# Kernel tuning notes

Measured on AMD Instinct MI355X. Metric: run time of the kernel, lower is better.

## Reference

```python
import jax, jax.numpy as jnp
import numpy as np

# hyperparameters (match init_kwargs)
LS = 0.2; GAMMA = 2.0; THING_W = 2.0; L_DB = 0.1; SIGMA = 0.05; TEMP = 0.1
L_DISTILL = 1.0; L_BPL = 0.5; L_ALIGN = 5.0; L_PROTO = 0.5; L_ENT = 0.3
L_IU = 0.5; L_IB = 0.5
MIN_PIX = 25; NUM_IDS = 24  # instance ids in [0, NUM_IDS)


def setup_inputs() -> dict:
    key = jax.random.key(0)
    k0, k1, k2, k3, k4 = jax.random.split(key, 5)
    B, C, H, W, D = 4, 27, 160, 160, 768
    return {
        "logits": jax.random.normal(k0, (B, C, H, W), jnp.float32),
        "cause_logits": jax.random.normal(k1, (B, C, H, W), jnp.float32),
        "dinov2_features": jax.random.normal(k2, (B, D, H, W), jnp.float32),
        "depth": jax.random.uniform(k3, (B, 1, H, W), jnp.float32),
        "instance_map": jax.random.randint(k4, (B, 1, H, W), 0, NUM_IDS),
    }


def _bce(x, y):
    x = jnp.clip(x, 1e-6, 1.0 - 1e-6)
    return -(y * jnp.log(x) + (1.0 - y) * jnp.log1p(-x)).mean()


def _forward(logits, cause_logits, dinov2_features, depth, instance_map):
    B, C, H, W = logits.shape
    logp = jax.nn.log_softmax(logits, axis=1)
    probs = jnp.exp(logp)

    # ---- distill: label-smoothed CE vs CAUSE hard labels, focal + thing + depth-boundary weights
    cause_labels = jnp.argmax(cause_logits, axis=1)  # (B,H,W)
    nll = -jnp.take_along_axis(logp, cause_labels[:, None], axis=1)[:, 0]  # (B,H,W)
    ce = (1.0 - LS) * nll + LS * (-logp.mean(axis=1))
    pt = jnp.exp(-jax.lax.stop_gradient(ce))
    w = (1.0 - pt) ** GAMMA
    thing = (cause_labels >= 11) & (cause_labels <= 18)
    w = jnp.where(thing, w * THING_W, w)
    gh = jnp.pad(jnp.abs(depth[:, :, 1:, :] - depth[:, :, :-1, :]), ((0, 0), (0, 0), (0, 1), (0, 0)))
    gw = jnp.pad(jnp.abs(depth[:, :, :, 1:] - depth[:, :, :, :-1]), ((0, 0), (0, 0), (0, 0), (0, 1)))
    gmag = (gh + gw)[:, 0]  # (B,H,W)
    gnorm = gmag / (gmag.mean() + 1e-6)
    w = w * (1.0 + L_DB * jnp.minimum(gnorm, 3.0))
    l_distill = (ce * w).mean()

    # ---- boundary preservation loss (CE re-weighted at pseudo-label boundaries)
    pl = jnp.pad(cause_labels, ((0, 0), (1, 1), (1, 1)), mode="edge")
    boundary = ((cause_labels != pl[:, 1:-1, 2:]) | (cause_labels != pl[:, 1:-1, :-2]) |
                (cause_labels != pl[:, 2:, 1:-1]) | (cause_labels != pl[:, :-2, 1:-1])).astype(jnp.float32)
    bsum = boundary.sum()
    l_bpl = jnp.where(bsum > 0, (ce * boundary).sum() / jnp.maximum(bsum, 1.0), 0.0)

    # ---- depth-boundary alignment
    two_s2 = 2.0 * SIGMA ** 2
    ddh = jnp.abs(depth[:, :, :, 1:] - depth[:, :, :, :-1])
    wh = jnp.exp(-(ddh ** 2) / two_s2)
    pdh = ((probs[:, :, :, 1:] - probs[:, :, :, :-1]) ** 2).sum(axis=1, keepdims=True)
    ddv = jnp.abs(depth[:, :, 1:, :] - depth[:, :, :-1, :])
    wv = jnp.exp(-(ddv ** 2) / two_s2)
    pdv = ((probs[:, :, 1:, :] - probs[:, :, :-1, :]) ** 2).sum(axis=1, keepdims=True)
    l_align = (wh * pdh).mean() + (wv * pdv).mean()

    # ---- feature prototype loss
    N = H * W
    probs_t = jax.nn.softmax(logits / TEMP, axis=1).reshape(B, C, N)   # (B,C,N)
    feats = dinov2_features.reshape(B, -1, N)                          # (B,D,N)
    protos = jnp.einsum("bdn,bcn->bdc", feats, probs_t)               # (B,D,C)
    wsum = probs_t.sum(axis=2)[:, None, :]                             # (B,1,C)
    protos = protos / (wsum + 1e-6)
    protos_n = protos / jnp.maximum(jnp.linalg.norm(protos, axis=1, keepdims=True), 1e-12)
    feats_n = feats / jnp.maximum(jnp.linalg.norm(feats, axis=1, keepdims=True), 1e-12)
    sim = jnp.einsum("bdc,bdn->bcn", protos_n, feats_n)               # (B,C,N)
    l_proto = -(probs_t * sim).sum() / (B * N)

    # ---- entropy loss
    l_ent = -(probs * logp).sum(axis=1).mean()

    # ---- instance boundary loss
    dh = jnp.abs(probs[:, :, 1:, :] - probs[:, :, :-1, :]).max(axis=1)
    dw = jnp.abs(probs[:, :, :, 1:] - probs[:, :, :, :-1]).max(axis=1)
    inst = instance_map[:, 0].astype(jnp.float32)
    th = (inst[:, 1:, :] != inst[:, :-1, :]).astype(jnp.float32)
    tw = (inst[:, :, 1:] != inst[:, :, :-1]).astype(jnp.float32)
    l_ib = (_bce(dh, th) + _bce(dw, tw)) / 2.0

    # ---- instance uniformity loss (vectorized segment reduce over instance ids)
    ids = instance_map[:, 0].reshape(B, N)                             # (B,N) int
    onehot = (ids[:, :, None] == jnp.arange(NUM_IDS)[None, None, :]).astype(jnp.float32)  # (B,N,K)
    counts = onehot.sum(axis=1)                                        # (B,K)
    pf = probs.reshape(B, C, N)
    s1 = jnp.einsum("bcn,bnk->bkc", pf, onehot)                       # per-id sum of probs
    s2 = jnp.einsum("bcn,bnk->bkc", pf * pf, onehot)                  # per-id sum of probs^2
    nc = jnp.maximum(counts, 1.0)[:, :, None]
    var = (s2 / nc - (s1 / nc) ** 2).mean(axis=2)                     # (B,K): mean over C of within-id variance
    valid = ((jnp.arange(NUM_IDS)[None, :] > 0) & (counts >= MIN_PIX)).astype(jnp.float32)
    l_iu = (var * valid).sum() / jnp.maximum(valid.sum(), 1.0)

    total = (L_DISTILL * l_distill + L_BPL * l_bpl + L_ALIGN * l_align +
             L_PROTO * l_proto + L_ENT * l_ent + L_IU * l_iu + L_IB * l_ib)
    return total


def reference(logits, cause_logits, dinov2_features, depth, instance_map):
    return _forward(logits, cause_logits, dinov2_features, depth, instance_map)
```

## Files before the change

### kernel.cpp

```cpp
#include <hip/hip_runtime.h>
#include <cstdint>
#include <cstddef>

#define BN 4
#define CC 27
#define HH 160
#define WW 160
#define HWp (HH*WW)
#define NPIX (BN*HWp)
#define DD 768
#define KK 24
#define NT 400
#define NTS 20
#define NSP 20
#define NPH (NTS/2)
#define GEMMB (BN*6*NSP)
#define TAILB (NPIX/256)

#define OFF_ACC 0
#define OFF_S1 32
#define OFF_S2 (OFF_S1+2592)
#define OFF_CNT (OFF_S2+2592)
#define ZERO_N (OFF_CNT+96)
#define OFF_NSQ8 ZERO_N
#define OFF_LAB (OFF_NSQ8 + 8*NPIX)
#define OFF_PROBS (OFF_LAB + NPIX/4)
#define OFF_PP (OFF_PROBS + BN*CC*HWp/2)
#define OFF_QP (OFF_PP + NSP*BN*CC*DD)
#define OFF_FBF (OFF_QP + NSP*BN*CC*DD)
#define OFF_WBF (OFF_FBF + (size_t)BN*6*NT*8192/4)

typedef __attribute__((ext_vector_type(4))) float f32x4;

__device__ __forceinline__ float wave_sum(float v) {
#pragma unroll
  for (int o = 32; o > 0; o >>= 1) v += __shfl_down(v, o, 64);
  return v;
}

__device__ __forceinline__ unsigned char f2fp8(float x) {
  return (unsigned char)(__builtin_amdgcn_cvt_pk_fp8_f32(x, x, 0, false) & 0xff);
}
__device__ __forceinline__ unsigned short f2bf(float x) {
  unsigned u = __builtin_bit_cast(unsigned, x);
  unsigned r = u + 0x7FFFu + ((u >> 16) & 1u);
  return (unsigned short)(r >> 16);
}
__device__ __forceinline__ float bf2f(unsigned short u) {
  unsigned v = ((unsigned)u) << 16;
  return __builtin_bit_cast(float, v);
}

__global__ void k_zero(float* __restrict__ w, int n) {
  int i = blockIdx.x * 256 + threadIdx.x;
  if (i < n) w[i] = 0.f;
}

__global__ void __launch_bounds__(256) k_prefconv(const float* __restrict__ feats,
        const float* __restrict__ depth, const float* __restrict__ cl,
        unsigned char* __restrict__ fbf, float* __restrict__ nsq8,
        unsigned char* __restrict__ lab, float* __restrict__ acc) {
  int t = threadIdx.x;
  if (blockIdx.x < 800) {
    int fcid = blockIdx.x;
    int slab = fcid % 100;
    int y = fcid / 100;
    int b = slab / (HWp / 1024);
    int px0 = (slab % (HWp / 1024)) * 1024;
    int d0 = y * (DD / 8);
    int p = px0 + 4 * t;
    int T = p >> 6, j = p & 63;
    const float* src = feats + ((size_t)b * DD + d0) * HWp + p;
    float n0 = 0.f, n1 = 0.f, n2 = 0.f, n3 = 0.f;
#pragma unroll 4
    for (int d = 0; d < DD / 8; ++d) {
      int dgl = d0 + d;
      float4 v = *(const float4*)(src + (size_t)d * HWp);
      n0 += v.x * v.x; n1 += v.y * v.y; n2 += v.z * v.z; n3 += v.w * v.w;
      int pk = __builtin_amdgcn_cvt_pk_fp8_f32(v.x, v.y, 0, false);
      pk = __builtin_amdgcn_cvt_pk_fp8_f32(v.z, v.w, pk, true);
      int dt = dgl >> 7, rin = dgl & 127;
      size_t addr = ((size_t)(b * 6 + dt) * NT + T) * 8192 + rin * 64
                  + (((j >> 3) ^ (rin & 7)) * 8) + (j & 7);
      *(int*)&fbf[addr] = pk;
    }
    float* nq = nsq8 + (size_t)y * NPIX + b * HWp + p;
    nq[0] = n0; nq[1] = n1; nq[2] = n2; nq[3] = n3;
  } else {
    int i = (blockIdx.x - 800) * 256 + t;
    float g = 0.f;
    {
      int b = i / HWp, r = i % HWp, h = r / WW, w = r % WW;
      const float* dp = depth + b * HWp;
      float d0 = dp[r];
      float gh = (h < HH-1) ? fabsf(dp[r+WW] - d0) : 0.f;
      float gw = (w < WW-1) ? fabsf(dp[r+1] - d0) : 0.f;
      g = gh + gw;
      const float* p = cl + (size_t)b * CC * HWp + r;
      float best = p[0]; int bi = 0;
#pragma unroll
      for (int c = 1; c < CC; ++c) {
        float v = p[(size_t)c * HWp];
        if (v > best) { best = v; bi = c; }
      }
      lab[i] = (unsigned char)bi;
    }
    __shared__ float red;
    if (t == 0) red = 0.f;
    __syncthreads();
    float s = wave_sum(g);
    if ((t & 63) == 0) atomicAdd(&red, s);
    __syncthreads();
    if (t == 0) atomicAdd(&acc[0], red);
  }
}

__global__ void k_main(const float* __restrict__ logits, const float* __restrict__ depth,
                       const unsigned char* __restrict__ lab, const float* __restrict__ nsq8,
                       unsigned short* __restrict__ probs, unsigned char* __restrict__ wbf,
                       float* __restrict__ acc) {
  int i = blockIdx.x * 256 + threadIdx.x;
  float c_dist = 0.f, c_bnum = 0.f, c_bcnt = 0.f, c_ent = 0.f;
  {
    int b = i / HWp, r = i % HWp, h = r / WW, w = r % WW;
    const float* lg = logits + (size_t)b * CC * HWp + r;
    float x[CC];
    float m = -1e30f;
#pragma unroll
    for (int c = 0; c < CC; ++c) { x[c] = lg[(size_t)c * HWp]; m = fmaxf(m, x[c]); }
    float se = 0.f, sx = 0.f, set = 0.f;
#pragma unroll
    for (int c = 0; c < CC; ++c) {
      se += expf(x[c] - m);
      set += expf(10.f * (x[c] - m));
      sx += x[c];
    }
    float lse = logf(se);
    float inv_set = 1.f / set;
    float ns = 0.f;
#pragma unroll
    for (int y = 0; y < 8; ++y) ns += nsq8[(size_t)y * NPIX + i];
    float invn = 1.f / fmaxf(sqrtf(ns), 1e-12f);
    int l = lab[i];
    float xl = x[0];
    float ent = 0.f;
    unsigned short* pb = probs + (size_t)b * CC * HWp + r;
    int T = r >> 6, j = r & 63;
    unsigned char* wb = wbf + ((size_t)b * NT + T) * 4096;
#pragma unroll
    for (int c = 0; c < CC; ++c) {
      float lp = x[c] - m - lse;
      float p = expf(lp);
      pb[(size_t)c * HWp] = f2bf(p);
      float ptc = expf(10.f * (x[c] - m)) * inv_set;
      wb[c * 64 + (((j >> 3) ^ (c & 7)) * 8) + (j & 7)] = f2fp8(ptc);
      int c2 = 32 + c;
      wb[c2 * 64 + (((j >> 3) ^ (c2 & 7)) * 8) + (j & 7)] = f2fp8(ptc * invn);
      ent -= p * lp;
      if (c == l) xl = x[c];
    }
    float nll = m + lse - xl;
    float ce = 0.8f * nll + 0.2f * (m + lse - sx * (1.f / CC));
    float ptf = expf(-ce);
    float wgt = (1.f - ptf) * (1.f - ptf);
    if (l >= 11 && l <= 18) wgt *= 2.f;
    const float* dp = depth + b * HWp;
    float d0 = dp[r];
    float gh = (h < HH-1) ? fabsf(dp[r+WW] - d0) : 0.f;
    float gw = (w < WW-1) ? fabsf(dp[r+1] - d0) : 0.f;
    float gmean = acc[0] * (1.f / NPIX);
    float gnorm = (gh + gw) / (gmean + 1e-6f);
    wgt *= 1.f + 0.1f * fminf(gnorm, 3.f);
    const unsigned char* lb = lab + b * HWp;
    int lL = lb[h*WW + (w>0 ? w-1 : w)];
    int lR = lb[h*WW + (w<WW-1 ? w+1 : w)];
    int lU = lb[(h>0 ? h-1 : h)*WW + w];
    int lD = lb[(h<HH-1 ? h+1 : h)*WW + w];
    float bnd = ((l != lL) | (l != lR) | (l != lU) | (l != lD)) ? 1.f : 0.f;
    c_dist = ce * wgt;
    c_bnum = ce * bnd;
    c_bcnt = bnd;
    c_ent = ent;
  }
  __shared__ float red[4];
  if (threadIdx.x < 4) red[threadIdx.x] = 0.f;
  __syncthreads();
  c_dist = wave_sum(c_dist); c_bnum = wave_sum(c_bnum);
  c_bcnt = wave_sum(c_bcnt); c_ent = wave_sum(c_ent);
  if ((threadIdx.x & 63) == 0) {
    atomicAdd(&red[0], c_dist); atomicAdd(&red[1], c_bnum);
    atomicAdd(&red[2], c_bcnt); atomicAdd(&red[3], c_ent);
  }
  __syncthreads();
  if (threadIdx.x == 0) {
    atomicAdd(&acc[1], red[0]); atomicAdd(&acc[2], red[1]);
    atomicAdd(&acc[3], red[2]); atomicAdd(&acc[4], red[3]);
  }
}

__global__ void __launch_bounds__(256) k_gemmtail(const unsigned char* __restrict__ fbf,
        const unsigned char* __restrict__ wbf,
        float* __restrict__ Pp, float* __restrict__ Qp,
        const unsigned short* __restrict__ probs, const float* __restrict__ depth,
        const int* __restrict__ inst, float* __restrict__ acc,
        float* __restrict__ s1g, float* __restrict__ s2g, float* __restrict__ cntg) {
  __shared__ __align__(16) unsigned char smem[73728];
  int t = threadIdx.x;
  if (blockIdx.x < GEMMB) {
    unsigned char (*As)[2][8192] = (unsigned char (*)[2][8192])smem;
    unsigned char (*Ws)[2][4096] = (unsigned char (*)[2][4096])(smem + 49152);
    int orig = blockIdx.x;
    int bx = (orig & 7) * 60 + (orig >> 3);
    int s  = bx % NSP;
    int dt = (bx / NSP) % 6;
    int b  = bx / (NSP * 6);
    int wave = t >> 6, lane = t & 63;
    int g = lane >> 4, rr = lane & 15;
    f32x4 acc4[2][4] = {};
    const unsigned char* Abase = fbf + ((size_t)(b*6+dt)*NT + s*NTS) * 8192;
    const unsigned char* Wbase = wbf + ((size_t)b*NT + s*NTS) * 4096;

#define STAGE2(ph, bufi) do { \
    _Pragma("unroll") \
    for (int c2_ = 0; c2_ < 2; ++c2_) { \
      const unsigned char* as_ = Abase + (size_t)((ph)*2 + c2_) * 8192; \
      const unsigned char* ws_ = Wbase + (size_t)((ph)*2 + c2_) * 4096; \
      _Pragma("unroll") \
      for (int i_ = 0; i_ < 2; ++i_) { \
        int off_ = wave*2048 + i_*1024; \
        __builtin_amdgcn_global_load_lds( \
          (const __attribute__((address_space(1))) void*)(as_ + off_ + lane*16), \
          (__attribute__((address_space(3))) void*)&As[bufi][c2_][off_], 16, 0, 0); \
      } \
      { \
        int off_ = wave*1024; \
        __builtin_amdgcn_global_load_lds( \
          (const __attribute__((address_space(1))) void*)(ws_ + off_ + lane*16), \
          (__attribute__((address_space(3))) void*)&Ws[bufi][c2_][off_], 16, 0, 0); \
      } \
    } \
  } while (0)

    STAGE2(0, 0);
    STAGE2(1, 1);
    int cur = 0;
    for (int ph = 0; ph < NPH; ++ph) {
      if (ph + 2 < NPH) {
        STAGE2(ph + 2, (cur + 2) % 3);
        asm volatile("s_waitcnt vmcnt(12)" ::: "memory");
      } else if (ph + 1 < NPH) {
        asm volatile("s_waitcnt vmcnt(6)" ::: "memory");
      } else {
        asm volatile("s_waitcnt vmcnt(0)" ::: "memory");
      }
      __builtin_amdgcn_s_barrier();
      __builtin_amdgcn_sched_barrier(0);
#pragma unroll
      for (int c2 = 0; c2 < 2; ++c2) {
#pragma unroll
        for (int ks = 0; ks < 2; ++ks) {
          long a[2]; long wf[4];
#pragma unroll
          for (int dd = 0; dd < 2; ++dd) {
            int row = (wave*2 + dd)*16 + rr;
            int ck = (ks*4 + g) ^ (row & 7);
            a[dd] = *(const long*)&As[cur][c2][row*64 + ck*8];
          }
#pragma unroll
          for (int ct = 0; ct < 4; ++ct) {
            int row = ct*16 + rr;
            int ck = (ks*4 + g) ^ (row & 7);
            wf[ct] = *(const long*)&Ws[cur][c2][row*64 + ck*8];
          }
#pragma unroll
          for (int dd = 0; dd < 2; ++dd)
#pragma unroll
            for (int ct = 0; ct < 4; ++ct)
              acc4[dd][ct] = __builtin_amdgcn_mfma_f32_16x16x32_fp8_fp8(a[dd], wf[ct], acc4[dd][ct], 0, 0, 0);
        }
      }
      __builtin_amdgcn_sched_barrier(0);
      __builtin_amdgcn_s_barrier();
      cur = (cur + 1) % 3;
    }
#undef STAGE2
#pragma unroll
    for (int dd = 0; dd < 2; ++dd) {
#pragma unroll
      for (int ct = 0; ct < 4; ++ct) {
        int cp = ct * 16 + rr;
        int d = dt * 128 + (wave * 2 + dd) * 16 + g * 4;
        f32x4 v = acc4[dd][ct];
        if (cp < CC)
          *(f32x4*)&Pp[(((size_t)s * BN + b) * CC + cp) * DD + d] = v;
        else if (cp >= 32 && cp < 32 + CC)
          *(f32x4*)&Qp[(((size_t)s * BN + b) * CC + (cp - 32)) * DD + d] = v;
      }
    }
  } else {
    float* ls1 = (float*)smem;
    float* ls2 = ls1 + 4*KK*CC;
    float* lc  = ls2 + 4*KK*CC;
    float* red = lc + 4*KK;
    int wv = t >> 6;
    for (int idx = t; idx < 4*KK*CC; idx += 256) { ls1[idx] = 0.f; ls2[idx] = 0.f; }
    if (t < 4*KK) lc[t] = 0.f;
    if (t < 4) red[t] = 0.f;
    __syncthreads();
    int i = (blockIdx.x - GEMMB) * 256 + t;
    int b = i / HWp, r = i % HWp, h = r / WW, w = r % WW;
    const unsigned short* P = probs + (size_t)b * CC * HWp + r;
    const int* ip = inst + b * HWp;
    int id = ip[r];
    atomicAdd(&lc[wv*KK + id], 1.f);
    bool hasR = (w < WW-1), hasD = (h < HH-1);
    float sh = 0.f, sv = 0.f, mh = 0.f, mw = 0.f;
#pragma unroll
    for (int c = 0; c < CC; ++c) {
      float p  = bf2f(P[(size_t)c * HWp]);
      atomicAdd(&ls1[(wv*KK + id)*CC + c], p);
      atomicAdd(&ls2[(wv*KK + id)*CC + c], p * p);
      float pr = hasR ? bf2f(P[(size_t)c * HWp + 1])  : p;
      float pd = hasD ? bf2f(P[(size_t)c * HWp + WW]) : p;
      float dr = pr - p, dd = pd - p;
      sh += dr * dr; sv += dd * dd;
      mw = fmaxf(mw, fabsf(dr)); mh = fmaxf(mh, fabsf(dd));
    }
    float aH = 0.f, aV = 0.f, bh = 0.f, bw = 0.f;
    const float* dp = depth + b * HWp;
    float d0 = dp[r];
    if (hasR) {
      float ddh = dp[r+1] - d0;
      aH = expf(-(ddh*ddh) * 200.f) * sh;
      float y = (ip[r+1] != ip[r]) ? 1.f : 0.f;
      float xx = fminf(fmaxf(mw, 1e-6f), 1.f - 1e-6f);
      bw = -(y * logf(xx) + (1.f - y) * log1pf(-xx));
    }
    if (hasD) {
      float ddv = dp[r+WW] - d0;
      aV = expf(-(ddv*ddv) * 200.f) * sv;
      float y = (ip[r+WW] != ip[r]) ? 1.f : 0.f;
      float xx = fminf(fmaxf(mh, 1e-6f), 1.f - 1e-6f);
      bh = -(y * logf(xx) + (1.f - y) * log1pf(-xx));
    }
    __syncthreads();
    aH = wave_sum(aH); aV = wave_sum(aV); bh = wave_sum(bh); bw = wave_sum(bw);
    if ((t & 63) == 0) {
      atomicAdd(&red[0], aH); atomicAdd(&red[1], aV);
      atomicAdd(&red[2], bh); atomicAdd(&red[3], bw);
    }
    __syncthreads();
    if (t == 0) {
      atomicAdd(&acc[5], red[0]); atomicAdd(&acc[6], red[1]);
      atomicAdd(&acc[7], red[2]); atomicAdd(&acc[8], red[3]);
    }
    for (int idx = t; idx < KK*CC; idx += 256) {
      atomicAdd(&s1g[b*KK*CC + idx], ls1[idx]+ls1[KK*CC+idx]+ls1[2*KK*CC+idx]+ls1[3*KK*CC+idx]);
      atomicAdd(&s2g[b*KK*CC + idx], ls2[idx]+ls2[KK*CC+idx]+ls2[2*KK*CC+idx]+ls2[3*KK*CC+idx]);
    }
    if (t < KK) atomicAdd(&cntg[b*KK + t], lc[t]+lc[KK+t]+lc[2*KK+t]+lc[3*KK+t]);
  }
}

__global__ void k_pfinal(const float* __restrict__ Pp, const float* __restrict__ Qp,
                         float* __restrict__ acc) {
  int bc = blockIdx.x;
  int b = bc / CC, c = bc % CC;
  float dot = 0.f, nsq = 0.f;
  for (int d = threadIdx.x; d < DD; d += 256) {
    float p = 0.f, q = 0.f;
#pragma unroll
    for (int s = 0; s < NSP; ++s) {
      size_t off = (((size_t)s * BN + b) * CC + c) * DD + d;
      p += Pp[off]; q += Qp[off];
    }
    dot += p * q; nsq += p * p;
  }
  __shared__ float red[2];
  if (threadIdx.x < 2) red[threadIdx.x] = 0.f;
  __syncthreads();
  dot = wave_sum(dot); nsq = wave_sum(nsq);
  if ((threadIdx.x & 63) == 0) { atomicAdd(&red[0], dot); atomicAdd(&red[1], nsq); }
  __syncthreads();
  if (threadIdx.x == 0) atomicAdd(&acc[9], red[0] / fmaxf(sqrtf(red[1]), 1e-12f));
}

__global__ void k_final(const float* __restrict__ s1g, const float* __restrict__ s2g,
                        const float* __restrict__ cntg, const float* __restrict__ acc,
                        float* __restrict__ out) {
  int t = threadIdx.x;
  float vsum = 0.f, vcnt = 0.f;
  if (t < BN*KK) {
    int k = t % KK;
    float count = cntg[t];
    float nc = fmaxf(count, 1.f);
    float var = 0.f;
#pragma unroll
    for (int c = 0; c < CC; ++c) {
      float m1 = s1g[t*CC + c] / nc;
      var += s2g[t*CC + c] / nc - m1 * m1;
    }
    var *= (1.f / CC);
    if (k > 0 && count >= 25.f) { vsum = var; vcnt = 1.f; }
  }
  __shared__ float red[2];
  if (t < 2) red[t] = 0.f;
  __syncthreads();
  vsum = wave_sum(vsum); vcnt = wave_sum(vcnt);
  if ((t & 63) == 0) { atomicAdd(&red[0], vsum); atomicAdd(&red[1], vcnt); }
  __syncthreads();
  if (t == 0) {
    float l_distill = acc[1] * (1.f / NPIX);
    float bcnt = acc[3];
    float l_bpl = (bcnt > 0.f) ? acc[2] / fmaxf(bcnt, 1.f) : 0.f;
    float l_align = acc[5] * (1.f / (BN*HH*(WW-1))) + acc[6] * (1.f / (BN*(HH-1)*WW));
    float l_ent = acc[4] * (1.f / NPIX);
    float l_ib = 0.5f * (acc[7] * (1.f / (BN*(HH-1)*WW)) + acc[8] * (1.f / (BN*HH*(WW-1))));
    float l_proto = -acc[9] * (1.f / NPIX);
    float l_iu = red[0] / fmaxf(red[1], 1.f);
    out[0] = 1.0f*l_distill + 0.5f*l_bpl + 5.0f*l_align + 0.5f*l_proto +
             0.3f*l_ent + 0.5f*l_iu + 0.5f*l_ib;
  }
}

extern "C" void kernel_launch(void* const* d_in, const int* in_sizes, int n_in,
                              void* d_out, int out_size, void* d_ws, size_t ws_size,
                              hipStream_t stream) {
  (void)in_sizes; (void)n_in; (void)out_size; (void)ws_size;
  const float* logits = (const float*)d_in[0];
  const float* cause  = (const float*)d_in[1];
  const float* feats  = (const float*)d_in[2];
  const float* depth  = (const float*)d_in[3];
  const int*   inst   = (const int*)d_in[4];
  float* ws = (float*)d_ws;
  float* acc = ws + OFF_ACC;
  float* s1  = ws + OFF_S1;
  float* s2  = ws + OFF_S2;
  float* cnt = ws + OFF_CNT;
  float* nsq8 = ws + OFF_NSQ8;
  float* Pp  = ws + OFF_PP;
  float* Qp  = ws + OFF_QP;
  unsigned char* lab = (unsigned char*)(ws + OFF_LAB);
  unsigned short* probs = (unsigned short*)(ws + OFF_PROBS);
  unsigned char* fbf = (unsigned char*)(ws + OFF_FBF);
  unsigned char* wbf = (unsigned char*)(ws + OFF_WBF);
  float* out = (float*)d_out;

  k_zero<<<(ZERO_N + 255) / 256, 256, 0, stream>>>(ws, ZERO_N);
  k_prefconv<<<1200, 256, 0, stream>>>(feats, depth, cause, fbf, nsq8, lab, acc);
  k_main<<<NPIX / 256, 256, 0, stream>>>(logits, depth, lab, nsq8, probs, wbf, acc);
  k_gemmtail<<<GEMMB + TAILB, 256, 0, stream>>>(fbf, wbf, Pp, Qp, probs, depth, inst,
                                                acc, s1, s2, cnt);
  k_pfinal<<<BN * CC, 256, 0, stream>>>(Pp, Qp, acc);
  k_final<<<1, 256, 0, stream>>>(s1, s2, cnt, acc, out);
}
```

Baseline: 194.7 us.

## Merge softmax prep into feature-conversion kernel and defer boundary/distill terms to tail

Puts the logits softmax, argmax labels, probs/ptc writes and entropy into the same launch as the fp8 feature conversion, so these pixel blocks run alongside the feature-conversion blocks. The distill and boundary terms, which need the global depth-gradient mean and the neighbour labels, move into the gemm tail through a new per-pixel CE buffer. A small new kernel computes the feature-norm-scaled ptc rows by re-reading the fp8 ptc values, which adds a second rounding step. Feature conversion now handles 8 pixels per thread with wider stores, and exp(10x) is replaced by powers of exp(x).

```diff
diff --git a/kernel.cpp b/kernel.cpp
--- a/kernel.cpp
+++ b/kernel.cpp
@@ -24,7 +24,8 @@
 #define ZERO_N (OFF_CNT+96)
 #define OFF_NSQ8 ZERO_N
 #define OFF_LAB (OFF_NSQ8 + 8*NPIX)
-#define OFF_PROBS (OFF_LAB + NPIX/4)
+#define OFF_CE (OFF_LAB + NPIX/4)
+#define OFF_PROBS (OFF_CE + NPIX)
 #define OFF_PP (OFF_PROBS + BN*CC*HWp/2)
 #define OFF_QP (OFF_PP + NSP*BN*CC*DD)
 #define OFF_FBF (OFF_QP + NSP*BN*CC*DD)
@@ -56,153 +57,134 @@
   if (i < n) w[i] = 0.f;
 }
 
-__global__ void __launch_bounds__(256) k_prefconv(const float* __restrict__ feats,
-        const float* __restrict__ depth, const float* __restrict__ cl,
+__global__ void __launch_bounds__(256) k_big(const float* __restrict__ feats,
+        const float* __restrict__ logits, const float* __restrict__ cause,
+        const float* __restrict__ depth,
         unsigned char* __restrict__ fbf, float* __restrict__ nsq8,
-        unsigned char* __restrict__ lab, float* __restrict__ acc) {
+        unsigned char* __restrict__ lab, float* __restrict__ ce_arr,
+        unsigned short* __restrict__ probs, unsigned char* __restrict__ wbf,
+        float* __restrict__ acc) {
   int t = threadIdx.x;
-  if (blockIdx.x < 800) {
+  if (blockIdx.x < 400) {
     int fcid = blockIdx.x;
-    int slab = fcid % 100;
-    int y = fcid / 100;
-    int b = slab / (HWp / 1024);
-    int px0 = (slab % (HWp / 1024)) * 1024;
-    int d0 = y * (DD / 8);
-    int p = px0 + 4 * t;
-    int T = p >> 6, j = p & 63;
-    const float* src = feats + ((size_t)b * DD + d0) * HWp + p;
-    float n0 = 0.f, n1 = 0.f, n2 = 0.f, n3 = 0.f;
+    int slab = fcid % 50;
+    int y = fcid / 50;
+    int i = slab * 2048 + 8 * t;
+    int b = i / HWp, r = i % HWp;
+    int T = r >> 6, chunk = (r & 63) >> 3;
+    const float* src0 = feats + ((size_t)b * DD + y * 96) * HWp + r;
+    float n[8] = {0,0,0,0,0,0,0,0};
 #pragma unroll 4
-    for (int d = 0; d < DD / 8; ++d) {
-      int dgl = d0 + d;
-      float4 v = *(const float4*)(src + (size_t)d * HWp);
-      n0 += v.x * v.x; n1 += v.y * v.y; n2 += v.z * v.z; n3 += v.w * v.w;
-      int pk = __builtin_amdgcn_cvt_pk_fp8_f32(v.x, v.y, 0, false);
-      pk = __builtin_amdgcn_cvt_pk_fp8_f32(v.z, v.w, pk, true);
+    for (int d = 0; d < 96; ++d) {
+      int dgl = y * 96 + d;
+      const float* src = src0 + (size_t)d * HWp;
+      float4 v0 = *(const float4*)src;
+      float4 v1 = *(const float4*)(src + 4);
+      n[0]+=v0.x*v0.x; n[1]+=v0.y*v0.y; n[2]+=v0.z*v0.z; n[3]+=v0.w*v0.w;
+      n[4]+=v1.x*v1.x; n[5]+=v1.y*v1.y; n[6]+=v1.z*v1.z; n[7]+=v1.w*v1.w;
+      int pk0 = __builtin_amdgcn_cvt_pk_fp8_f32(v0.x, v0.y, 0, false);
+      pk0 = __builtin_amdgcn_cvt_pk_fp8_f32(v0.z, v0.w, pk0, true);
+      int pk1 = __builtin_amdgcn_cvt_pk_fp8_f32(v1.x, v1.y, 0, false);
+      pk1 = __builtin_amdgcn_cvt_pk_fp8_f32(v1.z, v1.w, pk1, true);
       int dt = dgl >> 7, rin = dgl & 127;
       size_t addr = ((size_t)(b * 6 + dt) * NT + T) * 8192 + rin * 64
-                  + (((j >> 3) ^ (rin & 7)) * 8) + (j & 7);
-      *(int*)&fbf[addr] = pk;
-    }
-    float* nq = nsq8 + (size_t)y * NPIX + b * HWp + p;
-    nq[0] = n0; nq[1] = n1; nq[2] = n2; nq[3] = n3;
+                  + ((chunk ^ (rin & 7)) * 8);
+      int2 pk = make_int2(pk0, pk1);
+      *(int2*)&fbf[addr] = pk;
+    }
+    float* nq = nsq8 + (size_t)y * NPIX + i;
+    *(float4*)nq = make_float4(n[0], n[1], n[2], n[3]);
+    *(float4*)(nq + 4) = make_float4(n[4], n[5], n[6], n[7]);
   } else {
-    int i = (blockIdx.x - 800) * 256 + t;
-    float g = 0.f;
+    int i = (blockIdx.x - 400) * 256 + t;
+    int b = i / HWp, r = i % HWp, h = r / WW, w = r % WW;
+    float x[CC];
     {
-      int b = i / HWp, r = i % HWp, h = r / WW, w = r % WW;
+      const float* cp = cause + (size_t)b * CC * HWp + r;
+      float best = -1e30f; int bi = 0;
+#pragma unroll
+      for (int c = 0; c < CC; ++c) {
+        float v = cp[(size_t)c * HWp];
+        if (v > best) { best = v; bi = c; }
+      }
+      lab[i] = (unsigned char)bi;
+      const float* lg = logits + (size_t)b * CC * HWp + r;
+      float m = -1e30f;
+#pragma unroll
+      for (int c = 0; c < CC; ++c) { x[c] = lg[(size_t)c * HWp]; m = fmaxf(m, x[c]); }
+      float sx = 0.f, xl = 0.f;
+#pragma unroll
+      for (int c = 0; c < CC; ++c) { sx += x[c]; if (c == bi) xl = x[c]; }
+      float se = 0.f, set = 0.f, u = 0.f;
+#pragma unroll
+      for (int c = 0; c < CC; ++c) {
+        float tc = x[c] - m;
+        float e = expf(tc);
+        se += e; u += e * tc;
+        float e2 = e * e, e4 = e2 * e2;
+        set += e4 * e4 * e2;
+        x[c] = e;
+      }
+      float lse = logf(se);
+      float inv_se = 1.f / se, inv_set = 1.f / set;
+      float ent = lse - u * inv_se;
+      unsigned short* pb = probs + (size_t)b * CC * HWp + r;
+      int T = r >> 6, j = r & 63;
+      unsigned char* wb = wbf + ((size_t)b * NT + T) * 4096;
+#pragma unroll
+      for (int c = 0; c < CC; ++c) {
+        float e = x[c];
+        pb[(size_t)c * HWp] = f2bf(e * inv_se);
+        float e2 = e * e, e4 = e2 * e2;
+        float ptc = (e4 * e4 * e2) * inv_set;
+        wb[c * 64 + (((j >> 3) ^ (c & 7)) * 8) + (j & 7)] = f2fp8(ptc);
+      }
+      float ce = 0.8f * (m + lse - xl) + 0.2f * (m + lse - sx * (1.f / CC));
+      ce_arr[i] = ce;
       const float* dp = depth + b * HWp;
       float d0 = dp[r];
       float gh = (h < HH-1) ? fabsf(dp[r+WW] - d0) : 0.f;
       float gw = (w < WW-1) ? fabsf(dp[r+1] - d0) : 0.f;
-      g = gh + gw;
-      const float* p = cl + (size_t)b * CC * HWp + r;
-      float best = p[0]; int bi = 0;
-#pragma unroll
-      for (int c = 1; c < CC; ++c) {
-        float v = p[(size_t)c * HWp];
-        if (v > best) { best = v; bi = c; }
-      }
-      lab[i] = (unsigned char)bi;
-    }
-    __shared__ float red;
-    if (t == 0) red = 0.f;
-    __syncthreads();
-    float s = wave_sum(g);
-    if ((t & 63) == 0) atomicAdd(&red, s);
-    __syncthreads();
-    if (t == 0) atomicAdd(&acc[0], red);
-  }
-}
-
-__global__ void k_main(const float* __restrict__ logits, const float* __restrict__ depth,
-                       const unsigned char* __restrict__ lab, const float* __restrict__ nsq8,
-                       unsigned short* __restrict__ probs, unsigned char* __restrict__ wbf,
-                       float* __restrict__ acc) {
-  int i = blockIdx.x * 256 + threadIdx.x;
-  float c_dist = 0.f, c_bnum = 0.f, c_bcnt = 0.f, c_ent = 0.f;
-  {
-    int b = i / HWp, r = i % HWp, h = r / WW, w = r % WW;
-    const float* lg = logits + (size_t)b * CC * HWp + r;
-    float x[CC];
-    float m = -1e30f;
-#pragma unroll
-    for (int c = 0; c < CC; ++c) { x[c] = lg[(size_t)c * HWp]; m = fmaxf(m, x[c]); }
-    float se = 0.f, sx = 0.f, set = 0.f;
-#pragma unroll
-    for (int c = 0; c < CC; ++c) {
-      se += expf(x[c] - m);
-      set += expf(10.f * (x[c] - m));
-      sx += x[c];
-    }
-    float lse = logf(se);
-    float inv_set = 1.f / set;
-    float ns = 0.f;
-#pragma unroll
-    for (int y = 0; y < 8; ++y) ns += nsq8[(size_t)y * NPIX + i];
-    float invn = 1.f / fmaxf(sqrtf(ns), 1e-12f);
-    int l = lab[i];
-    float xl = x[0];
-    float ent = 0.f;
-    unsigned short* pb = probs + (size_t)b * CC * HWp + r;
-    int T = r >> 6, j = r & 63;
-    unsigned char* wb = wbf + ((size_t)b * NT + T) * 4096;
-#pragma unroll
-    for (int c = 0; c < CC; ++c) {
-      float lp = x[c] - m - lse;
-      float p = expf(lp);
-      pb[(size_t)c * HWp] = f2bf(p);
-      float ptc = expf(10.f * (x[c] - m)) * inv_set;
-      wb[c * 64 + (((j >> 3) ^ (c & 7)) * 8) + (j & 7)] = f2fp8(ptc);
-      int c2 = 32 + c;
-      wb[c2 * 64 + (((j >> 3) ^ (c2 & 7)) * 8) + (j & 7)] = f2fp8(ptc * invn);
-      ent -= p * lp;
-      if (c == l) xl = x[c];
-    }
-    float nll = m + lse - xl;
-    float ce = 0.8f * nll + 0.2f * (m + lse - sx * (1.f / CC));
-    float ptf = expf(-ce);
-    float wgt = (1.f - ptf) * (1.f - ptf);
-    if (l >= 11 && l <= 18) wgt *= 2.f;
-    const float* dp = depth + b * HWp;
-    float d0 = dp[r];
-    float gh = (h < HH-1) ? fabsf(dp[r+WW] - d0) : 0.f;
-    float gw = (w < WW-1) ? fabsf(dp[r+1] - d0) : 0.f;
-    float gmean = acc[0] * (1.f / NPIX);
-    float gnorm = (gh + gw) / (gmean + 1e-6f);
-    wgt *= 1.f + 0.1f * fminf(gnorm, 3.f);
-    const unsigned char* lb = lab + b * HWp;
-    int lL = lb[h*WW + (w>0 ? w-1 : w)];
-    int lR = lb[h*WW + (w<WW-1 ? w+1 : w)];
-    int lU = lb[(h>0 ? h-1 : h)*WW + w];
-    int lD = lb[(h<HH-1 ? h+1 : h)*WW + w];
-    float bnd = ((l != lL) | (l != lR) | (l != lU) | (l != lD)) ? 1.f : 0.f;
-    c_dist = ce * wgt;
-    c_bnum = ce * bnd;
-    c_bcnt = bnd;
-    c_ent = ent;
-  }
-  __shared__ float red[4];
-  if (threadIdx.x < 4) red[threadIdx.x] = 0.f;
-  __syncthreads();
-  c_dist = wave_sum(c_dist); c_bnum = wave_sum(c_bnum);
-  c_bcnt = wave_sum(c_bcnt); c_ent = wave_sum(c_ent);
-  if ((threadIdx.x & 63) == 0) {
-    atomicAdd(&red[0], c_dist); atomicAdd(&red[1], c_bnum);
-    atomicAdd(&red[2], c_bcnt); atomicAdd(&red[3], c_ent);
-  }
-  __syncthreads();
-  if (threadIdx.x == 0) {
-    atomicAdd(&acc[1], red[0]); atomicAdd(&acc[2], red[1]);
-    atomicAdd(&acc[3], red[2]); atomicAdd(&acc[4], red[3]);
-  }
+      float g = gh + gw;
+      __shared__ float red[2];
+      if (t < 2) red[t] = 0.f;
+      __syncthreads();
+      g = wave_sum(g); float es = wave_sum(ent);
+      if ((t & 63) == 0) { atomicAdd(&red[0], g); atomicAdd(&red[1], es); }
+      __syncthreads();
+      if (t == 0) { atomicAdd(&acc[0], red[0]); atomicAdd(&acc[4], red[1]); }
+    }
+  }
+}
+
+__global__ void __launch_bounds__(256) k_mainB(const float* __restrict__ nsq8,
+        unsigned char* __restrict__ wbf) {
+  int t = threadIdx.x;
+  int tt = blockIdx.x * 4 + (t >> 6);
+  int j = t & 63;
+  int b = tt / NT, T = tt % NT;
+  int i = b * HWp + T * 64 + j;
+  float ns = 0.f;
+#pragma unroll
+  for (int y = 0; y < 8; ++y) ns += nsq8[(size_t)y * NPIX + i];
+  float invn = 1.f / fmaxf(sqrtf(ns), 1e-12f);
+  unsigned char* wb = wbf + ((size_t)b * NT + T) * 4096;
+  int base = (((j >> 3)) * 8) + (j & 7);
+#pragma unroll
+  for (int c = 0; c < CC; ++c) {
+    int a1 = c * 64 + ((((j >> 3) ^ (c & 7))) * 8) + (j & 7);
+    float f = __builtin_amdgcn_cvt_f32_fp8((int)wb[a1], 0);
+    wb[a1 + 32 * 64] = f2fp8(f * invn);
+  }
+  (void)base;
 }
 
 __global__ void __launch_bounds__(256) k_gemmtail(const unsigned char* __restrict__ fbf,
         const unsigned char* __restrict__ wbf,
         float* __restrict__ Pp, float* __restrict__ Qp,
         const unsigned short* __restrict__ probs, const float* __restrict__ depth,
-        const int* __restrict__ inst, float* __restrict__ acc,
+        const int* __restrict__ inst, const unsigned char* __restrict__ lab,
+        const float* __restrict__ ce_arr, float* __restrict__ acc,
         float* __restrict__ s1g, float* __restrict__ s2g, float* __restrict__ cntg) {
   __shared__ __align__(16) unsigned char smem[73728];
   int t = threadIdx.x;
@@ -305,7 +287,7 @@
     int wv = t >> 6;
     for (int idx = t; idx < 4*KK*CC; idx += 256) { ls1[idx] = 0.f; ls2[idx] = 0.f; }
     if (t < 4*KK) lc[t] = 0.f;
-    if (t < 4) red[t] = 0.f;
+    if (t < 7) red[t] = 0.f;
     __syncthreads();
     int i = (blockIdx.x - GEMMB) * 256 + t;
     int b = i / HWp, r = i % HWp, h = r / WW, w = r % WW;
@@ -326,11 +308,13 @@
       sh += dr * dr; sv += dd * dd;
       mw = fmaxf(mw, fabsf(dr)); mh = fmaxf(mh, fabsf(dd));
     }
-    float aH = 0.f, aV = 0.f, bh = 0.f, bw = 0.f;
     const float* dp = depth + b * HWp;
     float d0 = dp[r];
+    float aH = 0.f, aV = 0.f, bh = 0.f, bw = 0.f;
+    float gh = 0.f, gw = 0.f;
     if (hasR) {
       float ddh = dp[r+1] - d0;
+      gw = fabsf(ddh);
       aH = expf(-(ddh*ddh) * 200.f) * sh;
       float y = (ip[r+1] != ip[r]) ? 1.f : 0.f;
       float xx = fminf(fmaxf(mw, 1e-6f), 1.f - 1e-6f);
@@ -338,21 +322,40 @@
     }
     if (hasD) {
       float ddv = dp[r+WW] - d0;
+      gh = fabsf(ddv);
       aV = expf(-(ddv*ddv) * 200.f) * sv;
       float y = (ip[r+WW] != ip[r]) ? 1.f : 0.f;
       float xx = fminf(fmaxf(mh, 1e-6f), 1.f - 1e-6f);
       bh = -(y * logf(xx) + (1.f - y) * log1pf(-xx));
     }
+    float ce = ce_arr[i];
+    int l = lab[i];
+    float ptf = expf(-ce);
+    float wgt = (1.f - ptf) * (1.f - ptf);
+    if (l >= 11 && l <= 18) wgt *= 2.f;
+    float gmean = acc[0] * (1.f / NPIX);
+    float gnorm = (gh + gw) / (gmean + 1e-6f);
+    wgt *= 1.f + 0.1f * fminf(gnorm, 3.f);
+    const unsigned char* lb = lab + b * HWp;
+    int lL = lb[h*WW + (w>0 ? w-1 : w)];
+    int lR = lb[h*WW + (w<WW-1 ? w+1 : w)];
+    int lU = lb[(h>0 ? h-1 : h)*WW + w];
+    int lD = lb[(h<HH-1 ? h+1 : h)*WW + w];
+    float bnd = ((l != lL) | (l != lR) | (l != lU) | (l != lD)) ? 1.f : 0.f;
+    float c_dist = ce * wgt, c_bnum = ce * bnd, c_bcnt = bnd;
     __syncthreads();
     aH = wave_sum(aH); aV = wave_sum(aV); bh = wave_sum(bh); bw = wave_sum(bw);
+    c_dist = wave_sum(c_dist); c_bnum = wave_sum(c_bnum); c_bcnt = wave_sum(c_bcnt);
     if ((t & 63) == 0) {
       atomicAdd(&red[0], aH); atomicAdd(&red[1], aV);
       atomicAdd(&red[2], bh); atomicAdd(&red[3], bw);
+      atomicAdd(&red[4], c_dist); atomicAdd(&red[5], c_bnum); atomicAdd(&red[6], c_bcnt);
     }
     __syncthreads();
     if (t == 0) {
       atomicAdd(&acc[5], red[0]); atomicAdd(&acc[6], red[1]);
       atomicAdd(&acc[7], red[2]); atomicAdd(&acc[8], red[3]);
+      atomicAdd(&acc[1], red[4]); atomicAdd(&acc[2], red[5]); atomicAdd(&acc[3], red[6]);
     }
     for (int idx = t; idx < KK*CC; idx += 256) {
       atomicAdd(&s1g[b*KK*CC + idx], ls1[idx]+ls1[KK*CC+idx]+ls1[2*KK*CC+idx]+ls1[3*KK*CC+idx]);
@@ -438,6 +441,7 @@
   float* s2  = ws + OFF_S2;
   float* cnt = ws + OFF_CNT;
   float* nsq8 = ws + OFF_NSQ8;
+  float* ce  = ws + OFF_CE;
   float* Pp  = ws + OFF_PP;
   float* Qp  = ws + OFF_QP;
   unsigned char* lab = (unsigned char*)(ws + OFF_LAB);
@@ -447,10 +451,11 @@
   float* out = (float*)d_out;
 
   k_zero<<<(ZERO_N + 255) / 256, 256, 0, stream>>>(ws, ZERO_N);
-  k_prefconv<<<1200, 256, 0, stream>>>(feats, depth, cause, fbf, nsq8, lab, acc);
-  k_main<<<NPIX / 256, 256, 0, stream>>>(logits, depth, lab, nsq8, probs, wbf, acc);
+  k_big<<<800, 256, 0, stream>>>(feats, logits, cause, depth, fbf, nsq8, lab, ce,
+                                 probs, wbf, acc);
+  k_mainB<<<400, 256, 0, stream>>>(nsq8, wbf);
   k_gemmtail<<<GEMMB + TAILB, 256, 0, stream>>>(fbf, wbf, Pp, Qp, probs, depth, inst,
-                                                acc, s1, s2, cnt);
+                                                lab, ce, acc, s1, s2, cnt);
   k_pfinal<<<BN * CC, 256, 0, stream>>>(Pp, Qp, acc);
   k_final<<<1, 256, 0, stream>>>(s1, s2, cnt, acc, out);
 }
```

Result: no change. 191.1 us (-1.8%).
